# Performance work log

Measured on AMD Instinct MI355X. Metric: run time of the kernel, lower is better.

The kernel has to match this reference:

```python
import jax, jax.numpy as jnp
import numpy as np

POSE_DIM = 16
H_DIM = 32
SEQ_LEN = 25
BATCH = 262144


def setup_inputs() -> dict:
    key = jax.random.key(0)
    ks = jax.random.split(key, 9)
    s = 0.1  # keep gates out of saturation
    return {
        "first_input": jax.random.normal(ks[0], (BATCH, POSE_DIM), dtype=jnp.float32),
        "h0": jax.random.normal(ks[1], (BATCH, H_DIM), dtype=jnp.float32),
        "c0": jax.random.normal(ks[2], (BATCH, H_DIM), dtype=jnp.float32),
        # LSTM params, torch layout/gate order (i, f, g, o)
        "W_ih": s * jax.random.normal(ks[3], (4 * H_DIM, POSE_DIM), dtype=jnp.float32),
        "W_hh": s * jax.random.normal(ks[4], (4 * H_DIM, H_DIM), dtype=jnp.float32),
        "b_ih": s * jax.random.normal(ks[5], (4 * H_DIM,), dtype=jnp.float32),
        "b_hh": s * jax.random.normal(ks[6], (4 * H_DIM,), dtype=jnp.float32),
        # hidden -> input-space projection
        "W_out": s * jax.random.normal(ks[7], (POSE_DIM, H_DIM), dtype=jnp.float32),
        "b_out": s * jax.random.normal(ks[8], (POSE_DIM,), dtype=jnp.float32),
    }


def reference(first_input, h0, c0, W_ih, W_hh, b_ih, b_hh, W_out, b_out):
    # Gate order matches torch.nn.LSTM: i, f, g, o.
    b = b_ih + b_hh  # [4H]

    def step(carry, _):
        x, h, c = carry  # x: [B, P], h/c: [B, H]
        gates = x @ W_ih.T + h @ W_hh.T + b  # [B, 4H]
        i, f, g, o = jnp.split(gates, 4, axis=-1)
        c = jax.nn.sigmoid(f) * c + jax.nn.sigmoid(i) * jnp.tanh(g)
        h = jax.nn.sigmoid(o) * jnp.tanh(c)
        x_next = h @ W_out.T + b_out  # projected back to pose space [B, P]
        return (x_next, h, c), x_next

    _, preds = jax.lax.scan(step, (first_input, h0, c0), None, length=SEQ_LEN)
    # preds: [S, B, P] -> [B, S, P] to match torch cat along dim=1
    return jnp.transpose(preds, (1, 0, 2))
```

## Files before the change

kernel.cpp:

```cpp
#include <hip/hip_runtime.h>
#include <hip/hip_bf16.h>


constexpr int P = 16;
constexpr int H = 32;
constexpr int S = 25;

typedef short        bf16x8 __attribute__((ext_vector_type(8)));
typedef float        f32x16 __attribute__((ext_vector_type(16)));
typedef float        f32x4  __attribute__((ext_vector_type(4)));
typedef unsigned int u32x4  __attribute__((ext_vector_type(4)));

union FragU { u32x4 u; bf16x8 b; };

__device__ __forceinline__ unsigned int pkbf(float lo, float hi) {
    unsigned short a = __builtin_bit_cast(unsigned short, __float2bfloat16(lo));
    unsigned short b = __builtin_bit_cast(unsigned short, __float2bfloat16(hi));
    return (unsigned int)a | ((unsigned int)b << 16);
}

__device__ __forceinline__ float sigf(float v) {
    return __builtin_amdgcn_rcpf(1.0f + __expf(-v));
}
__device__ __forceinline__ float tanh_fast(float v) {
    return 1.0f - 2.0f * __builtin_amdgcn_rcpf(1.0f + __expf(2.0f * v));
}

__global__ void setup_frags(const float* __restrict__ Wih, const float* __restrict__ Whh,
                            const float* __restrict__ bih, const float* __restrict__ bhh,
                            const float* __restrict__ Wout, const float* __restrict__ bout,
                            unsigned int* __restrict__ ws)
{
    auto waug = [&](int r, int k) -> float {
        if (r < 128) {
            if (k < 32) {
                float a = Whh[r * H + k];
                for (int p = 0; p < P; ++p) a += Wih[r * P + p] * Wout[p * H + k];
                return a;
            }
            if (k == 32) {
                float a = bih[r] + bhh[r];
                for (int p = 0; p < P; ++p) a += Wih[r * P + p] * bout[p];
                return a;
            }
            return 0.0f;
        } else if (r < 144) {
            int p = r - 128;
            if (k < 32)  return Wout[p * H + k];
            if (k == 32) return bout[p];
            return 0.0f;
        }
        return 0.0f;
    };
    auto w0aug = [&](int r, int k) -> float {
        if (k < 16) return Wih[r * P + k];
        if (k < 48) return Whh[r * H + (k - 16)];
        if (k == 48) return bih[r] + bhh[r];
        return 0.0f;
    };

    const int tid = threadIdx.x;
    for (int idx = tid; idx < 5 * 3 * 64 * 4; idx += 256) {
        int v = idx & 3, l = (idx >> 2) & 63, tc = idx >> 8;
        int t = tc / 3, c = tc % 3;
        int r = 32 * t + (l & 31);
        int k = 16 * c + 8 * (l >> 5) + 2 * v;
        ws[idx] = pkbf(waug(r, k), waug(r, k + 1));
    }
    for (int idx = tid; idx < 4 * 4 * 64 * 4; idx += 256) {
        int v = idx & 3, l = (idx >> 2) & 63, tc = idx >> 8;
        int t = tc / 4, c = tc % 4;
        int r = 32 * t + (l & 31);
        int k = 16 * c + 8 * (l >> 5) + 2 * v;
        ws[3840 + idx] = pkbf(w0aug(r, k), w0aug(r, k + 1));
    }
}

__global__ __launch_bounds__(256, 2) void decoder_mfma(
    const float* __restrict__ x0, const float* __restrict__ h0,
    const float* __restrict__ c0, const unsigned int* __restrict__ ws,
    float* __restrict__ out, int batch)
{
    const int lane = threadIdx.x & 63;
    const int wid  = threadIdx.x >> 6;
    const int bcol = lane & 31;
    const int hi   = lane >> 5;
    const int bg   = (blockIdx.x * 4 + wid) * 32 + bcol;
    if (bg >= batch) return;

    FragU A[5][3];
    #pragma unroll
    for (int t = 0; t < 5; ++t)
        #pragma unroll
        for (int c = 0; c < 3; ++c)
            A[t][c].u = *reinterpret_cast<const u32x4*>(ws + ((t * 3 + c) * 64 + lane) * 4);

    FragU Bbias;
    Bbias.u.x = (hi == 0) ? 0x3F80u : 0u;
    Bbias.u.y = 0u; Bbias.u.z = 0u; Bbias.u.w = 0u;

    float cc[16];
    #pragma unroll
    for (int q = 0; q < 4; ++q) {
        f32x4 t = *reinterpret_cast<const f32x4*>(c0 + (size_t)bg * H + q * 8 + 4 * hi);
        cc[q * 4 + 0] = t.x; cc[q * 4 + 1] = t.y; cc[q * 4 + 2] = t.z; cc[q * 4 + 3] = t.w;
    }

    const f32x16 vzero = {};
    f32x16 acc[4];

    {
        FragU B0[4];
        {
            const float* p = x0 + (size_t)bg * P + 8 * hi;
            f32x4 a = *reinterpret_cast<const f32x4*>(p);
            f32x4 b = *reinterpret_cast<const f32x4*>(p + 4);
            B0[0].u.x = pkbf(a.x, a.y); B0[0].u.y = pkbf(a.z, a.w);
            B0[0].u.z = pkbf(b.x, b.y); B0[0].u.w = pkbf(b.z, b.w);
        }
        #pragma unroll
        for (int cch = 0; cch < 2; ++cch) {
            const float* p = h0 + (size_t)bg * H + 16 * cch + 8 * hi;
            f32x4 a = *reinterpret_cast<const f32x4*>(p);
            f32x4 b = *reinterpret_cast<const f32x4*>(p + 4);
            B0[1 + cch].u.x = pkbf(a.x, a.y); B0[1 + cch].u.y = pkbf(a.z, a.w);
            B0[1 + cch].u.z = pkbf(b.x, b.y); B0[1 + cch].u.w = pkbf(b.z, b.w);
        }
        B0[3] = Bbias;

        #pragma unroll
        for (int t = 0; t < 4; ++t) acc[t] = vzero;
        #pragma unroll
        for (int c4 = 0; c4 < 4; ++c4) {
            #pragma unroll
            for (int t = 0; t < 4; ++t) {
                FragU a;
                a.u = *reinterpret_cast<const u32x4*>(ws + 3840 + ((t * 4 + c4) * 64 + lane) * 4);
                acc[t] = __builtin_amdgcn_mfma_f32_32x32x16_bf16(a.b, B0[c4].b, acc[t], 0, 0, 0);
            }
        }
    }

    FragU Bh[2];
    for (int s = 0; s < S; ++s) {
        float hreg[16];
        #pragma unroll
        for (int r = 0; r < 16; ++r) {
            float gi = acc[0][r], gf = acc[1][r], gg = acc[2][r], go = acc[3][r];
            float cn = sigf(gf) * cc[r] + sigf(gi) * tanh_fast(gg);
            cc[r] = cn;
            hreg[r] = sigf(go) * tanh_fast(cn);
        }

        unsigned int w[8], pw[8];
        #pragma unroll
        for (int q = 0; q < 4; ++q) {
            w[2 * q]     = pkbf(hreg[4 * q + 0], hreg[4 * q + 1]);
            w[2 * q + 1] = pkbf(hreg[4 * q + 2], hreg[4 * q + 3]);
        }
        #pragma unroll
        for (int i = 0; i < 8; ++i) pw[i] = __shfl_xor(w[i], 32);
        Bh[0].u.x = hi ? pw[2] : w[0];  Bh[0].u.y = hi ? pw[3] : w[1];
        Bh[0].u.z = hi ? w[2]  : pw[0]; Bh[0].u.w = hi ? w[3]  : pw[1];
        Bh[1].u.x = hi ? pw[6] : w[4];  Bh[1].u.y = hi ? pw[7] : w[5];
        Bh[1].u.z = hi ? w[6]  : pw[4]; Bh[1].u.w = hi ? w[7]  : pw[5];

        f32x16 px = vzero;
        px = __builtin_amdgcn_mfma_f32_32x32x16_bf16(A[4][0].b, Bh[0].b,  px, 0, 0, 0);
        px = __builtin_amdgcn_mfma_f32_32x32x16_bf16(A[4][1].b, Bh[1].b,  px, 0, 0, 0);
        px = __builtin_amdgcn_mfma_f32_32x32x16_bf16(A[4][2].b, Bbias.b, px, 0, 0, 0);

        float* op = out + ((size_t)bg * S + s) * P + 4 * hi;
        f32x4 v0; v0.x = px[0]; v0.y = px[1]; v0.z = px[2]; v0.w = px[3];
        f32x4 v1; v1.x = px[4]; v1.y = px[5]; v1.z = px[6]; v1.w = px[7];
        __builtin_nontemporal_store(v0, reinterpret_cast<f32x4*>(op));
        __builtin_nontemporal_store(v1, reinterpret_cast<f32x4*>(op + 8));

        if (s + 1 < S) {
            #pragma unroll
            for (int t = 0; t < 4; ++t) acc[t] = vzero;
            #pragma unroll
            for (int cch = 0; cch < 2; ++cch)
                #pragma unroll
                for (int t = 0; t < 4; ++t)
                    acc[t] = __builtin_amdgcn_mfma_f32_32x32x16_bf16(A[t][cch].b, Bh[cch].b, acc[t], 0, 0, 0);
            #pragma unroll
            for (int t = 0; t < 4; ++t)
                acc[t] = __builtin_amdgcn_mfma_f32_32x32x16_bf16(A[t][2].b, Bbias.b, acc[t], 0, 0, 0);
        }
    }
}

extern "C" void kernel_launch(void* const* d_in, const int* in_sizes, int n_in,
                              void* d_out, int out_size, void* d_ws, size_t ws_size,
                              hipStream_t stream) {
    const float* x0   = (const float*)d_in[0];
    const float* h0   = (const float*)d_in[1];
    const float* c0   = (const float*)d_in[2];
    const float* Wih  = (const float*)d_in[3];
    const float* Whh  = (const float*)d_in[4];
    const float* bih  = (const float*)d_in[5];
    const float* bhh  = (const float*)d_in[6];
    const float* Wout = (const float*)d_in[7];
    const float* bout = (const float*)d_in[8];
    float* out = (float*)d_out;
    unsigned int* ws = (unsigned int*)d_ws;

    const int batch = in_sizes[0] / P;

    hipLaunchKernelGGL(setup_frags, dim3(1), dim3(256), 0, stream,
                       Wih, Whh, bih, bhh, Wout, bout, ws);

    dim3 block(256);
    dim3 grid((batch + 127) / 128);
    hipLaunchKernelGGL(decoder_mfma, grid, block, 0, stream,
                       x0, h0, c0, ws, out, batch);
}
```

Measured before the change: 260.9 us.

## Fold gate exp scaling into weights, permute K layout to drop cross-lane shuffles

Pre-scales the gate weight rows by -log2(e), or -2log2(e) for the g gate, so the kernel can use raw exp2 on MFMA outputs. Sigmoid and tanh pairs are merged so they share one reciprocal each. The K index permutation in the weight fragments matches the accumulator row layout, so h can be packed directly into B fragments without the __shfl_xor exchange and selects. The bias MFMA is issued first so it can start before the activations finish. This reduces transcendental and shuffle work per step, at the cost of possible overflow in the merged reciprocal products for large gate values.

```diff
diff --git a/kernel.cpp b/kernel.cpp
--- a/kernel.cpp
+++ b/kernel.cpp
@@ -13,17 +13,21 @@
 
 union FragU { u32x4 u; bf16x8 b; };
 
+#if __has_builtin(__builtin_amdgcn_exp2f)
+#define EX2 __builtin_amdgcn_exp2f
+#else
+#define EX2 exp2f
+#endif
+
 __device__ __forceinline__ unsigned int pkbf(float lo, float hi) {
     unsigned short a = __builtin_bit_cast(unsigned short, __float2bfloat16(lo));
     unsigned short b = __builtin_bit_cast(unsigned short, __float2bfloat16(hi));
     return (unsigned int)a | ((unsigned int)b << 16);
 }
 
-__device__ __forceinline__ float sigf(float v) {
-    return __builtin_amdgcn_rcpf(1.0f + __expf(-v));
-}
-__device__ __forceinline__ float tanh_fast(float v) {
-    return 1.0f - 2.0f * __builtin_amdgcn_rcpf(1.0f + __expf(2.0f * v));
+__device__ __forceinline__ float gate_scale(int r) {
+    return (r >= 64 && r < 96) ? -2.8853900817779268f
+                               : -1.4426950408889634f;
 }
 
 __global__ void setup_frags(const float* __restrict__ Wih, const float* __restrict__ Whh,
@@ -32,16 +36,17 @@
                             unsigned int* __restrict__ ws)
 {
     auto waug = [&](int r, int k) -> float {
+        float s = (r < 128) ? gate_scale(r) : 1.0f;
         if (r < 128) {
             if (k < 32) {
                 float a = Whh[r * H + k];
                 for (int p = 0; p < P; ++p) a += Wih[r * P + p] * Wout[p * H + k];
-                return a;
+                return s * a;
             }
             if (k == 32) {
                 float a = bih[r] + bhh[r];
                 for (int p = 0; p < P; ++p) a += Wih[r * P + p] * bout[p];
-                return a;
+                return s * a;
             }
             return 0.0f;
         } else if (r < 144) {
@@ -53,9 +58,10 @@
         return 0.0f;
     };
     auto w0aug = [&](int r, int k) -> float {
-        if (k < 16) return Wih[r * P + k];
-        if (k < 48) return Whh[r * H + (k - 16)];
-        if (k == 48) return bih[r] + bhh[r];
+        float s = gate_scale(r);
+        if (k < 16)  return s * Wih[r * P + k];
+        if (k < 48)  return s * Whh[r * H + (k - 16)];
+        if (k == 48) return s * (bih[r] + bhh[r]);
         return 0.0f;
     };
 
@@ -64,14 +70,14 @@
         int v = idx & 3, l = (idx >> 2) & 63, tc = idx >> 8;
         int t = tc / 3, c = tc % 3;
         int r = 32 * t + (l & 31);
-        int k = 16 * c + 8 * (l >> 5) + 2 * v;
+        int k = 16 * c + 8 * (v >> 1) + 4 * (l >> 5) + 2 * (v & 1);
         ws[idx] = pkbf(waug(r, k), waug(r, k + 1));
     }
     for (int idx = tid; idx < 4 * 4 * 64 * 4; idx += 256) {
         int v = idx & 3, l = (idx >> 2) & 63, tc = idx >> 8;
         int t = tc / 4, c = tc % 4;
         int r = 32 * t + (l & 31);
-        int k = 16 * c + 8 * (l >> 5) + 2 * v;
+        int k = 16 * c + 8 * (v >> 1) + 4 * (l >> 5) + 2 * (v & 1);
         ws[3840 + idx] = pkbf(w0aug(r, k), w0aug(r, k + 1));
     }
 }
@@ -112,19 +118,19 @@
     {
         FragU B0[4];
         {
-            const float* p = x0 + (size_t)bg * P + 8 * hi;
-            f32x4 a = *reinterpret_cast<const f32x4*>(p);
-            f32x4 b = *reinterpret_cast<const f32x4*>(p + 4);
-            B0[0].u.x = pkbf(a.x, a.y); B0[0].u.y = pkbf(a.z, a.w);
-            B0[0].u.z = pkbf(b.x, b.y); B0[0].u.w = pkbf(b.z, b.w);
-        }
-        #pragma unroll
-        for (int cch = 0; cch < 2; ++cch) {
-            const float* p = h0 + (size_t)bg * H + 16 * cch + 8 * hi;
-            f32x4 a = *reinterpret_cast<const f32x4*>(p);
-            f32x4 b = *reinterpret_cast<const f32x4*>(p + 4);
-            B0[1 + cch].u.x = pkbf(a.x, a.y); B0[1 + cch].u.y = pkbf(a.z, a.w);
-            B0[1 + cch].u.z = pkbf(b.x, b.y); B0[1 + cch].u.w = pkbf(b.z, b.w);
+            const float* p = x0 + (size_t)bg * P;
+            f32x4 a  = *reinterpret_cast<const f32x4*>(p + 4 * hi);
+            f32x4 b4 = *reinterpret_cast<const f32x4*>(p + 8 + 4 * hi);
+            B0[0].u.x = pkbf(a.x, a.y);  B0[0].u.y = pkbf(a.z, a.w);
+            B0[0].u.z = pkbf(b4.x, b4.y); B0[0].u.w = pkbf(b4.z, b4.w);
+        }
+        #pragma unroll
+        for (int ch = 0; ch < 2; ++ch) {
+            const float* p = h0 + (size_t)bg * H + 16 * ch;
+            f32x4 a  = *reinterpret_cast<const f32x4*>(p + 4 * hi);
+            f32x4 b4 = *reinterpret_cast<const f32x4*>(p + 8 + 4 * hi);
+            B0[1 + ch].u.x = pkbf(a.x, a.y);  B0[1 + ch].u.y = pkbf(a.z, a.w);
+            B0[1 + ch].u.z = pkbf(b4.x, b4.y); B0[1 + ch].u.w = pkbf(b4.z, b4.w);
         }
         B0[3] = Bbias;
 
@@ -143,32 +149,32 @@
 
     FragU Bh[2];
     for (int s = 0; s < S; ++s) {
-        float hreg[16];
+        float hh[16];
         #pragma unroll
         for (int r = 0; r < 16; ++r) {
-            float gi = acc[0][r], gf = acc[1][r], gg = acc[2][r], go = acc[3][r];
-            float cn = sigf(gf) * cc[r] + sigf(gi) * tanh_fast(gg);
+            const float ei = EX2(acc[0][r]);
+            const float ef = EX2(acc[1][r]);
+            const float eg = EX2(acc[2][r]);
+            const float eo = EX2(acc[3][r]);
+            const float r1 = __builtin_amdgcn_rcpf((1.0f + ei) * (1.0f + eg));
+            const float tg = (1.0f - eg) * r1;
+            const float rf = __builtin_amdgcn_rcpf(1.0f + ef);
+            const float cn = __builtin_fmaf(cc[r], rf, tg);
             cc[r] = cn;
-            hreg[r] = sigf(go) * tanh_fast(cn);
-        }
-
-        unsigned int w[8], pw[8];
-        #pragma unroll
-        for (int q = 0; q < 4; ++q) {
-            w[2 * q]     = pkbf(hreg[4 * q + 0], hreg[4 * q + 1]);
-            w[2 * q + 1] = pkbf(hreg[4 * q + 2], hreg[4 * q + 3]);
-        }
-        #pragma unroll
-        for (int i = 0; i < 8; ++i) pw[i] = __shfl_xor(w[i], 32);
-        Bh[0].u.x = hi ? pw[2] : w[0];  Bh[0].u.y = hi ? pw[3] : w[1];
-        Bh[0].u.z = hi ? w[2]  : pw[0]; Bh[0].u.w = hi ? w[3]  : pw[1];
-        Bh[1].u.x = hi ? pw[6] : w[4];  Bh[1].u.y = hi ? pw[7] : w[5];
-        Bh[1].u.z = hi ? w[6]  : pw[4]; Bh[1].u.w = hi ? w[7]  : pw[5];
-
-        f32x16 px = vzero;
-        px = __builtin_amdgcn_mfma_f32_32x32x16_bf16(A[4][0].b, Bh[0].b,  px, 0, 0, 0);
-        px = __builtin_amdgcn_mfma_f32_32x32x16_bf16(A[4][1].b, Bh[1].b,  px, 0, 0, 0);
-        px = __builtin_amdgcn_mfma_f32_32x32x16_bf16(A[4][2].b, Bbias.b, px, 0, 0, 0);
+            const float ec = EX2(cn * -2.8853900817779268f);
+            const float r2 = __builtin_amdgcn_rcpf((1.0f + ec) * (1.0f + eo));
+            hh[r] = (1.0f - ec) * r2;
+        }
+
+        Bh[0].u.x = pkbf(hh[0],  hh[1]);  Bh[0].u.y = pkbf(hh[2],  hh[3]);
+        Bh[0].u.z = pkbf(hh[4],  hh[5]);  Bh[0].u.w = pkbf(hh[6],  hh[7]);
+        Bh[1].u.x = pkbf(hh[8],  hh[9]);  Bh[1].u.y = pkbf(hh[10], hh[11]);
+        Bh[1].u.z = pkbf(hh[12], hh[13]); Bh[1].u.w = pkbf(hh[14], hh[15]);
+
+        f32x16 px;
+        px = __builtin_amdgcn_mfma_f32_32x32x16_bf16(A[4][2].b, Bbias.b, vzero, 0, 0, 0);
+        px = __builtin_amdgcn_mfma_f32_32x32x16_bf16(A[4][0].b, Bh[0].b, px,    0, 0, 0);
+        px = __builtin_amdgcn_mfma_f32_32x32x16_bf16(A[4][1].b, Bh[1].b, px,    0, 0, 0);
 
         float* op = out + ((size_t)bg * S + s) * P + 4 * hi;
         f32x4 v0; v0.x = px[0]; v0.y = px[1]; v0.z = px[2]; v0.w = px[3];
@@ -178,15 +184,13 @@
 
         if (s + 1 < S) {
             #pragma unroll
-            for (int t = 0; t < 4; ++t) acc[t] = vzero;
+            for (int t = 0; t < 4; ++t)
+                acc[t] = __builtin_amdgcn_mfma_f32_32x32x16_bf16(A[t][2].b, Bbias.b, vzero, 0, 0, 0);
             #pragma unroll
-            for (int cch = 0; cch < 2; ++cch)
+            for (int ch = 0; ch < 2; ++ch)
                 #pragma unroll
                 for (int t = 0; t < 4; ++t)
-                    acc[t] = __builtin_amdgcn_mfma_f32_32x32x16_bf16(A[t][cch].b, Bh[cch].b, acc[t], 0, 0, 0);
-            #pragma unroll
-            for (int t = 0; t < 4; ++t)
-                acc[t] = __builtin_amdgcn_mfma_f32_32x32x16_bf16(A[t][2].b, Bbias.b, acc[t], 0, 0, 0);
+                    acc[t] = __builtin_amdgcn_mfma_f32_32x32x16_bf16(A[t][ch].b, Bh[ch].b, acc[t], 0, 0, 0);
         }
     }
 }
```

New measurement: 228.4 us. 1.14x faster.
